# Kernel optimization log

Measured on AMD Instinct MI355X. Metric: run time of the kernel, lower is better.

The kernel has to match this reference:

```python
import jax, jax.numpy as jnp
import numpy as np

B = 128          # number of graphs
N = 512          # nodes per graph
D = 128          # input_dim == hid_dim
H = 128          # hid_dim
L = 2            # num GIN layers
E_PG = 8192      # edges per graph (avg degree 16)
OUT = 10
BN_EPS = 1e-5
RATIO = 0.5


def setup_inputs() -> dict:
    key = jax.random.key(0)
    ks = jax.random.split(key, 32)
    NT = B * N
    # per-graph random edges, offset into the global node index space
    e = jax.random.randint(ks[0], (2, B, E_PG), 0, N)
    offs = (jnp.arange(B) * N)[None, :, None]
    edge_index = (e + offs).reshape(2, -1).astype(jnp.int64)
    batch = jnp.repeat(jnp.arange(B), N).astype(jnp.int64)
    x = jax.random.normal(ks[1], (NT, D), dtype=jnp.float32)
    sc = 0.05
    inp = {
        'x': x, 'edge_index': edge_index, 'batch': batch,
        'epss': jax.random.normal(ks[2], (L,), jnp.float32) * 0.1,
        'Ws1': jax.random.normal(ks[3], (L, D, 2 * H), jnp.float32) * sc,
        'bs1': jax.random.normal(ks[4], (L, 2 * H), jnp.float32) * sc,
        'g1s': jax.random.uniform(ks[5], (L, 2 * H), jnp.float32, 0.5, 1.5),
        'be1s': jax.random.normal(ks[6], (L, 2 * H), jnp.float32) * sc,
        'rm1s': jax.random.normal(ks[7], (L, 2 * H), jnp.float32) * 0.1,
        'rv1s': jax.random.uniform(ks[8], (L, 2 * H), jnp.float32, 0.5, 1.5),
        'Ws2': jax.random.normal(ks[9], (L, 2 * H, H), jnp.float32) * sc,
        'bs2': jax.random.normal(ks[10], (L, H), jnp.float32) * sc,
        'gbn': jax.random.uniform(ks[11], (L, H), jnp.float32, 0.5, 1.5),
        'bbn': jax.random.normal(ks[12], (L, H), jnp.float32) * sc,
        'rmbn': jax.random.normal(ks[13], (L, H), jnp.float32) * 0.1,
        'rvbn': jax.random.uniform(ks[14], (L, H), jnp.float32, 0.5, 1.5),
        'Wrel': jax.random.normal(ks[15], (H, 1), jnp.float32) * sc,
        'brel': jax.random.normal(ks[16], (1,), jnp.float32) * sc,
        'Wroot': jax.random.normal(ks[17], (H, 1), jnp.float32) * sc,
        'W_lin1': jax.random.normal(ks[18], (H, H), jnp.float32) * sc,
        'b_lin1': jax.random.normal(ks[19], (H,), jnp.float32) * sc,
        'g_h': jax.random.uniform(ks[20], (H,), jnp.float32, 0.5, 1.5),
        'be_h': jax.random.normal(ks[21], (H,), jnp.float32) * sc,
        'rm_h': jax.random.normal(ks[22], (H,), jnp.float32) * 0.1,
        'rv_h': jax.random.uniform(ks[23], (H,), jnp.float32, 0.5, 1.5),
        'W_lin2': jax.random.normal(ks[24], (H, OUT), jnp.float32) * sc,
        'b_lin2': jax.random.normal(ks[25], (OUT,), jnp.float32) * sc,
    }
    return inp


def _bn(h, g, b, rm, rv):
    # eval-mode BatchNorm1d
    return (h - rm) * jax.lax.rsqrt(rv + BN_EPS) * g + b


def _forward(x, edge_index, batch, epss, Ws1, bs1, g1s, be1s, rm1s, rv1s,
             Ws2, bs2, gbn, bbn, rmbn, rvbn, Wrel, brel, Wroot,
             W_lin1, b_lin1, g_h, be_h, rm_h, rv_h, W_lin2, b_lin2):
    NT = x.shape[0]
    src, dst = edge_index[0], edge_index[1]
    # ---- stacked GINConv + BN + ReLU (eval: dropout = identity) ----
    for l in range(L):
        agg = jax.ops.segment_sum(x[src], dst, num_segments=NT)   # scatter-add
        h = (1.0 + epss[l]) * x + agg
        h = h @ Ws1[l] + bs1[l]
        h = jax.nn.relu(_bn(h, g1s[l], be1s[l], rm1s[l], rv1s[l]))
        h = h @ Ws2[l] + bs2[l]
        x = jax.nn.relu(_bn(h, gbn[l], bbn[l], rmbn[l], rvbn[l]))
    # ---- SAGPooling: GraphConv score -> tanh -> per-graph top-k ----
    agg = jax.ops.segment_sum(x[src], dst, num_segments=NT)
    score = (agg @ Wrel + brel + x @ Wroot)[:, 0]                 # [NT]
    s = jnp.tanh(score)
    K = int(np.ceil(RATIO * N))
    vals, idx = jax.lax.top_k(s.reshape(B, N), K)                 # [B,K]
    perm = (idx + (jnp.arange(B) * N)[:, None]).reshape(-1)       # global node ids
    x_pool = x[perm] * vals.reshape(-1)[:, None]                  # [B*K, H]
    batch_pool = batch[perm]
    # ---- global add pool ----
    embedding = jax.ops.segment_sum(x_pool, batch_pool, num_segments=B)  # [B,H]
    # ---- head (B > 1 branch) ----
    h = _bn(embedding @ W_lin1 + b_lin1, g_h, be_h, rm_h, rv_h)
    h = jax.nn.relu(h)
    logits = h @ W_lin2 + b_lin2
    return embedding, logits


def reference(x, edge_index, batch, epss, Ws1, bs1, g1s, be1s, rm1s, rv1s,
              Ws2, bs2, gbn, bbn, rmbn, rvbn, Wrel, brel, Wroot,
              W_lin1, b_lin1, g_h, be_h, rm_h, rv_h, W_lin2, b_lin2):
    return _forward(x, edge_index, batch, epss, Ws1, bs1, g1s, be1s, rm1s,
                    rv1s, Ws2, bs2, gbn, bbn, rmbn, rvbn, Wrel, brel, Wroot,
                    W_lin1, b_lin1, g_h, be_h, rm_h, rv_h, W_lin2, b_lin2)
```

## Files before the change

kernel.cpp:

```cpp
#include <hip/hip_runtime.h>
#include <hip/hip_bf16.h>
#include <stdint.h>
#include <math.h>

#define NT_ 65536
#define BGRAPH 128
#define NNODE 512
#define DIM 128
#define HID 128
#define H2 256
#define EDGES 1048576
#define EPG 8192
#define KSEL 256
#define OUTC 10

typedef float v2f __attribute__((ext_vector_type(2)));

__global__ __launch_bounds__(512) void k_csr(const int* __restrict__ src, const int* __restrict__ dst,
                                             int* __restrict__ row_start, int* __restrict__ csr2) {
    __shared__ int hist[512];
    __shared__ int scan_s[512];
    __shared__ int cur[512];
    __shared__ int eids[EPG];
    const int g = blockIdx.x;
    const int t = threadIdx.x;
    const int base = g * EPG;
    const int nb = g * NNODE;
    hist[t] = 0;
    __syncthreads();
    #pragma unroll
    for (int j = t; j < EPG; j += 512) {
        int d = dst[base + j] - nb;
        atomicAdd(&hist[d], 1);
    }
    __syncthreads();
    int v = hist[t];
    scan_s[t] = v;
    __syncthreads();
    for (int off = 1; off < 512; off <<= 1) {
        int u = (t >= off) ? scan_s[t - off] : 0;
        __syncthreads();
        scan_s[t] += u;
        __syncthreads();
    }
    int excl = scan_s[t] - v;
    row_start[nb + t] = base + excl;
    cur[t] = excl;
    if (g == BGRAPH - 1 && t == 511) row_start[NT_] = EDGES;
    __syncthreads();
    #pragma unroll
    for (int j = t; j < EPG; j += 512) {
        int d = dst[base + j] - nb;
        int pos = atomicAdd(&cur[d], 1);
        eids[pos] = (d << 16) | j;
    }
    __syncthreads();
    #pragma unroll
    for (int p = t; p < EPG; p += 512) {
        int packed = eids[p];
        int j = packed & 0xFFFF;
        int d = packed >> 16;
        int beg = scan_s[d] - hist[d];
        int end = scan_s[d];
        int rank = 0;
        for (int q = beg; q < end; ++q) rank += (int)((eids[q] & 0xFFFF) < j);
        csr2[base + beg + rank] = src[base + j];
    }
}

__global__ __launch_bounds__(256) void k_aggcomb(const float* __restrict__ X,
        const int* __restrict__ row_start, const int* __restrict__ csr_src,
        const float* __restrict__ epss, int l, float* __restrict__ XIN) {
    int bid = blockIdx.x;
    int wg = (bid & 7) * 1024 + (bid >> 3);
    int wave = threadIdx.x >> 6;
    int lane = threadIdx.x & 63;
    int half = lane >> 5;
    int l32 = lane & 31;
    int n = wg * 8 + wave * 2 + half;
    int beg = row_start[n], end = row_start[n + 1];
    const size_t co = (size_t)(l32 * 4);
    const float ep = __fadd_rn(1.0f, epss[l]);
    float a0 = 0.f, a1 = 0.f, a2 = 0.f, a3 = 0.f;
    int p = beg;
    for (; p + 8 <= end; p += 8) {
        int n0 = csr_src[p+0], n1 = csr_src[p+1], n2 = csr_src[p+2], n3 = csr_src[p+3];
        int n4 = csr_src[p+4], n5 = csr_src[p+5], n6 = csr_src[p+6], n7 = csr_src[p+7];
        float4 v0 = *(const float4*)(X + (size_t)n0 * DIM + co);
        float4 v1 = *(const float4*)(X + (size_t)n1 * DIM + co);
        float4 v2 = *(const float4*)(X + (size_t)n2 * DIM + co);
        float4 v3 = *(const float4*)(X + (size_t)n3 * DIM + co);
        float4 v4 = *(const float4*)(X + (size_t)n4 * DIM + co);
        float4 v5 = *(const float4*)(X + (size_t)n5 * DIM + co);
        float4 v6 = *(const float4*)(X + (size_t)n6 * DIM + co);
        float4 v7 = *(const float4*)(X + (size_t)n7 * DIM + co);
        a0 = __fadd_rn(a0, v0.x); a1 = __fadd_rn(a1, v0.y); a2 = __fadd_rn(a2, v0.z); a3 = __fadd_rn(a3, v0.w);
        a0 = __fadd_rn(a0, v1.x); a1 = __fadd_rn(a1, v1.y); a2 = __fadd_rn(a2, v1.z); a3 = __fadd_rn(a3, v1.w);
        a0 = __fadd_rn(a0, v2.x); a1 = __fadd_rn(a1, v2.y); a2 = __fadd_rn(a2, v2.z); a3 = __fadd_rn(a3, v2.w);
        a0 = __fadd_rn(a0, v3.x); a1 = __fadd_rn(a1, v3.y); a2 = __fadd_rn(a2, v3.z); a3 = __fadd_rn(a3, v3.w);
        a0 = __fadd_rn(a0, v4.x); a1 = __fadd_rn(a1, v4.y); a2 = __fadd_rn(a2, v4.z); a3 = __fadd_rn(a3, v4.w);
        a0 = __fadd_rn(a0, v5.x); a1 = __fadd_rn(a1, v5.y); a2 = __fadd_rn(a2, v5.z); a3 = __fadd_rn(a3, v5.w);
        a0 = __fadd_rn(a0, v6.x); a1 = __fadd_rn(a1, v6.y); a2 = __fadd_rn(a2, v6.z); a3 = __fadd_rn(a3, v6.w);
        a0 = __fadd_rn(a0, v7.x); a1 = __fadd_rn(a1, v7.y); a2 = __fadd_rn(a2, v7.z); a3 = __fadd_rn(a3, v7.w);
    }
    for (; p < end; ++p) {
        int nbr = csr_src[p];
        float4 v = *(const float4*)(X + (size_t)nbr * DIM + co);
        a0 = __fadd_rn(a0, v.x); a1 = __fadd_rn(a1, v.y); a2 = __fadd_rn(a2, v.z); a3 = __fadd_rn(a3, v.w);
    }
    float4 xv = *(const float4*)(X + (size_t)n * DIM + co);
    float4 o;
    o.x = __fadd_rn(__fmul_rn(ep, xv.x), a0);
    o.y = __fadd_rn(__fmul_rn(ep, xv.y), a1);
    o.z = __fadd_rn(__fmul_rn(ep, xv.z), a2);
    o.w = __fadd_rn(__fmul_rn(ep, xv.w), a3);
    *(float4*)(XIN + (size_t)n * DIM + co) = o;
}

__global__ __launch_bounds__(256) void k_gemm1(const float* __restrict__ XIN,
        const float* __restrict__ Ws1, const float* __restrict__ bs1,
        const float* __restrict__ g1s, const float* __restrict__ be1s, const float* __restrict__ rm1s,
        const float* __restrict__ rv1s, int l, float* __restrict__ H1out) {
    __shared__ float As[2][16][132];
    __shared__ float Bs[2][16][132];
    const float* W1  = Ws1 + (size_t)l * DIM * H2;
    const float* b1  = bs1 + l * H2;
    const float* g1  = g1s + l * H2;
    const float* be1 = be1s + l * H2;
    const float* rm1 = rm1s + l * H2;
    const float* rv1 = rv1s + l * H2;
    int bid = blockIdx.x;
    int wg = (bid & 7) * 128 + (bid >> 3);
    const int mbase = (wg >> 1) * 128;
    const int nbase = (wg & 1) * 128;
    const int tid = threadIdx.x;
    const int srow = tid >> 1;
    const int sk   = (tid & 1) * 8;
    const int bk   = tid >> 4;
    const int bc   = (tid & 15) * 4;
    const int ty = tid >> 4;
    const int tx = tid & 15;
    v2f acc[8][4] = {};
    const float* xr = XIN + (size_t)(mbase + srow) * DIM + sk;
    float4 px0, px1, pw0, pw1;
    px0 = *(const float4*)(xr);     px1 = *(const float4*)(xr + 4);
    {
        const float* wrow = W1 + (size_t)bk * H2 + nbase;
        pw0 = *(const float4*)(wrow + bc); pw1 = *(const float4*)(wrow + bc + 64);
    }
    As[0][sk + 0][srow] = px0.x;
    As[0][sk + 1][srow] = px0.y;
    As[0][sk + 2][srow] = px0.z;
    As[0][sk + 3][srow] = px0.w;
    As[0][sk + 4][srow] = px1.x;
    As[0][sk + 5][srow] = px1.y;
    As[0][sk + 6][srow] = px1.z;
    As[0][sk + 7][srow] = px1.w;
    *(float4*)&Bs[0][bk][bc]      = pw0;
    *(float4*)&Bs[0][bk][bc + 64] = pw1;
    __syncthreads();
    int cur = 0;
    for (int kt = 0; kt < DIM; kt += 16) {
        const int nxt = kt + 16;
        if (nxt < DIM) {
            px0 = *(const float4*)(xr + nxt);     px1 = *(const float4*)(xr + nxt + 4);
            const float* wrow = W1 + (size_t)(nxt + bk) * H2 + nbase;
            pw0 = *(const float4*)(wrow + bc); pw1 = *(const float4*)(wrow + bc + 64);
        }
        #pragma unroll
        for (int kk = 0; kk < 16; ++kk) {
            const float4 aA = *(const float4*)&As[cur][kk][ty * 8];
            const float4 aB = *(const float4*)&As[cur][kk][ty * 8 + 4];
            const float4 b0 = *(const float4*)&Bs[cur][kk][tx * 4];
            const float4 b1v = *(const float4*)&Bs[cur][kk][tx * 4 + 64];
            v2f b00; b00[0] = b0.x;  b00[1] = b0.y;
            v2f b01; b01[0] = b0.z;  b01[1] = b0.w;
            v2f b10; b10[0] = b1v.x; b10[1] = b1v.y;
            v2f b11; b11[0] = b1v.z; b11[1] = b1v.w;
            const float arr[8] = {aA.x, aA.y, aA.z, aA.w, aB.x, aB.y, aB.z, aB.w};
            #pragma unroll
            for (int i = 0; i < 8; ++i) {
                v2f ai; ai[0] = arr[i]; ai[1] = arr[i];
                acc[i][0] = __builtin_elementwise_fma(ai, b00, acc[i][0]);
                acc[i][1] = __builtin_elementwise_fma(ai, b01, acc[i][1]);
                acc[i][2] = __builtin_elementwise_fma(ai, b10, acc[i][2]);
                acc[i][3] = __builtin_elementwise_fma(ai, b11, acc[i][3]);
            }
        }
        if (nxt < DIM) {
            const int nb = cur ^ 1;
            As[nb][sk + 0][srow] = px0.x;
            As[nb][sk + 1][srow] = px0.y;
            As[nb][sk + 2][srow] = px0.z;
            As[nb][sk + 3][srow] = px0.w;
            As[nb][sk + 4][srow] = px1.x;
            As[nb][sk + 5][srow] = px1.y;
            As[nb][sk + 6][srow] = px1.z;
            As[nb][sk + 7][srow] = px1.w;
            *(float4*)&Bs[nb][bk][bc]      = pw0;
            *(float4*)&Bs[nb][bk][bc + 64] = pw1;
            __syncthreads();
        }
        cur ^= 1;
    }
    const int gc = nbase + tx * 4;
    float bb[8], iv[8], gg[8], rr[8], ee[8];
    #pragma unroll
    for (int j = 0; j < 8; ++j) {
        int c = (j < 4) ? (gc + j) : (gc + 60 + j);
        bb[j] = b1[c];
        iv[j] = __fdiv_rn(1.0f, __fsqrt_rn(__fadd_rn(rv1[c], 1e-5f)));
        gg[j] = g1[c];
        rr[j] = rm1[c];
        ee[j] = be1[c];
    }
    #pragma unroll
    for (int i = 0; i < 8; ++i) {
        const int gr = mbase + ty * 8 + i;
        float cv[8] = {acc[i][0][0], acc[i][0][1], acc[i][1][0], acc[i][1][1],
                       acc[i][2][0], acc[i][2][1], acc[i][3][0], acc[i][3][1]};
        float r[8];
        #pragma unroll
        for (int j = 0; j < 8; ++j) {
            float t = __fadd_rn(cv[j], bb[j]);
            t = __fsub_rn(t, rr[j]); t = __fmul_rn(t, iv[j]);
            t = __fmul_rn(t, gg[j]); t = __fadd_rn(t, ee[j]);
            r[j] = fmaxf(t, 0.f);
        }
        float4 o0; o0.x = r[0]; o0.y = r[1]; o0.z = r[2]; o0.w = r[3];
        float4 o1; o1.x = r[4]; o1.y = r[5]; o1.z = r[6]; o1.w = r[7];
        *(float4*)(H1out + (size_t)gr * H2 + gc)      = o0;
        *(float4*)(H1out + (size_t)gr * H2 + gc + 64) = o1;
    }
}

__global__ __launch_bounds__(256) void k_gemm2(const float* __restrict__ H1, const float* __restrict__ Ws2,
        const float* __restrict__ bs2, const float* __restrict__ gbn, const float* __restrict__ bbn,
        const float* __restrict__ rmbn, const float* __restrict__ rvbn, int l, float* __restrict__ Xout) {
    __shared__ float As[2][16][132];
    __shared__ float Bs[2][16][132];
    const float* W2 = Ws2 + (size_t)l * H2 * HID;
    const float* b2 = bs2 + l * HID;
    const float* g  = gbn + l * HID;
    const float* be = bbn + l * HID;
    const float* rm = rmbn + l * HID;
    const float* rv = rvbn + l * HID;
    int bid = blockIdx.x;
    int wg = (bid & 7) * 64 + (bid >> 3);
    const int mbase = wg * 128;
    const int tid = threadIdx.x;
    const int srow = tid >> 1;
    const int sk   = (tid & 1) * 8;
    const int bk   = tid >> 4;
    const int bc   = (tid & 15) * 4;
    const int ty = tid >> 4;
    const int tx = tid & 15;
    v2f acc[8][4] = {};
    const float* hr = H1 + (size_t)(mbase + srow) * H2 + sk;
    float4 ph0, ph1, pw0, pw1;
    ph0 = *(const float4*)(hr);     ph1 = *(const float4*)(hr + 4);
    {
        const float* wrow = W2 + (size_t)bk * HID;
        pw0 = *(const float4*)(wrow + bc); pw1 = *(const float4*)(wrow + bc + 64);
    }
    As[0][sk + 0][srow] = ph0.x;
    As[0][sk + 1][srow] = ph0.y;
    As[0][sk + 2][srow] = ph0.z;
    As[0][sk + 3][srow] = ph0.w;
    As[0][sk + 4][srow] = ph1.x;
    As[0][sk + 5][srow] = ph1.y;
    As[0][sk + 6][srow] = ph1.z;
    As[0][sk + 7][srow] = ph1.w;
    *(float4*)&Bs[0][bk][bc]      = pw0;
    *(float4*)&Bs[0][bk][bc + 64] = pw1;
    __syncthreads();
    int cur = 0;
    for (int kt = 0; kt < H2; kt += 16) {
        const int nxt = kt + 16;
        if (nxt < H2) {
            ph0 = *(const float4*)(hr + nxt);     ph1 = *(const float4*)(hr + nxt + 4);
            const float* wrow = W2 + (size_t)(nxt + bk) * HID;
            pw0 = *(const float4*)(wrow + bc); pw1 = *(const float4*)(wrow + bc + 64);
        }
        #pragma unroll
        for (int kk = 0; kk < 16; ++kk) {
            const float4 aA = *(const float4*)&As[cur][kk][ty * 8];
            const float4 aB = *(const float4*)&As[cur][kk][ty * 8 + 4];
            const float4 b0 = *(const float4*)&Bs[cur][kk][tx * 4];
            const float4 b1v = *(const float4*)&Bs[cur][kk][tx * 4 + 64];
            v2f b00; b00[0] = b0.x;  b00[1] = b0.y;
            v2f b01; b01[0] = b0.z;  b01[1] = b0.w;
            v2f b10; b10[0] = b1v.x; b10[1] = b1v.y;
            v2f b11; b11[0] = b1v.z; b11[1] = b1v.w;
            const float arr[8] = {aA.x, aA.y, aA.z, aA.w, aB.x, aB.y, aB.z, aB.w};
            #pragma unroll
            for (int i = 0; i < 8; ++i) {
                v2f ai; ai[0] = arr[i]; ai[1] = arr[i];
                acc[i][0] = __builtin_elementwise_fma(ai, b00, acc[i][0]);
                acc[i][1] = __builtin_elementwise_fma(ai, b01, acc[i][1]);
                acc[i][2] = __builtin_elementwise_fma(ai, b10, acc[i][2]);
                acc[i][3] = __builtin_elementwise_fma(ai, b11, acc[i][3]);
            }
        }
        if (nxt < H2) {
            const int nb = cur ^ 1;
            As[nb][sk + 0][srow] = ph0.x;
            As[nb][sk + 1][srow] = ph0.y;
            As[nb][sk + 2][srow] = ph0.z;
            As[nb][sk + 3][srow] = ph0.w;
            As[nb][sk + 4][srow] = ph1.x;
            As[nb][sk + 5][srow] = ph1.y;
            As[nb][sk + 6][srow] = ph1.z;
            As[nb][sk + 7][srow] = ph1.w;
            *(float4*)&Bs[nb][bk][bc]      = pw0;
            *(float4*)&Bs[nb][bk][bc + 64] = pw1;
            __syncthreads();
        }
        cur ^= 1;
    }
    const int gc = tx * 4;
    float bb[8], iv[8], gg[8], rr[8], ee[8];
    #pragma unroll
    for (int j = 0; j < 8; ++j) {
        int c = (j < 4) ? (gc + j) : (gc + 60 + j);
        bb[j] = b2[c];
        iv[j] = __fdiv_rn(1.0f, __fsqrt_rn(__fadd_rn(rv[c], 1e-5f)));
        gg[j] = g[c];
        rr[j] = rm[c];
        ee[j] = be[c];
    }
    #pragma unroll
    for (int i = 0; i < 8; ++i) {
        const int gr = mbase + ty * 8 + i;
        float cv[8] = {acc[i][0][0], acc[i][0][1], acc[i][1][0], acc[i][1][1],
                       acc[i][2][0], acc[i][2][1], acc[i][3][0], acc[i][3][1]};
        float r[8];
        #pragma unroll
        for (int j = 0; j < 8; ++j) {
            float t = __fadd_rn(cv[j], bb[j]);
            t = __fsub_rn(t, rr[j]); t = __fmul_rn(t, iv[j]);
            t = __fmul_rn(t, gg[j]); t = __fadd_rn(t, ee[j]);
            r[j] = fmaxf(t, 0.f);
        }
        float4 o0; o0.x = r[0]; o0.y = r[1]; o0.z = r[2]; o0.w = r[3];
        float4 o1; o1.x = r[4]; o1.y = r[5]; o1.z = r[6]; o1.w = r[7];
        *(float4*)(Xout + (size_t)gr * HID + gc)      = o0;
        *(float4*)(Xout + (size_t)gr * HID + gc + 64) = o1;
    }
}

__global__ __launch_bounds__(256) void k_aggscore(const float* __restrict__ X,
        const int* __restrict__ row_start, const int* __restrict__ csr_src,
        const float* __restrict__ Wrel, const float* __restrict__ brel,
        const float* __restrict__ Wroot, float* __restrict__ S) {
    int bid = blockIdx.x;
    int wg = (bid & 7) * 1024 + (bid >> 3);
    int wave = threadIdx.x >> 6;
    int lane = threadIdx.x & 63;
    int half = lane >> 5;
    int l32 = lane & 31;
    int n = wg * 8 + wave * 2 + half;
    int beg = row_start[n], end = row_start[n + 1];
    const size_t co = (size_t)(l32 * 4);
    float a0 = 0.f, a1 = 0.f, a2 = 0.f, a3 = 0.f;
    int p = beg;
    for (; p + 8 <= end; p += 8) {
        int n0 = csr_src[p+0], n1 = csr_src[p+1], n2 = csr_src[p+2], n3 = csr_src[p+3];
        int n4 = csr_src[p+4], n5 = csr_src[p+5], n6 = csr_src[p+6], n7 = csr_src[p+7];
        float4 v0 = *(const float4*)(X + (size_t)n0 * DIM + co);
        float4 v1 = *(const float4*)(X + (size_t)n1 * DIM + co);
        float4 v2 = *(const float4*)(X + (size_t)n2 * DIM + co);
        float4 v3 = *(const float4*)(X + (size_t)n3 * DIM + co);
        float4 v4 = *(const float4*)(X + (size_t)n4 * DIM + co);
        float4 v5 = *(const float4*)(X + (size_t)n5 * DIM + co);
        float4 v6 = *(const float4*)(X + (size_t)n6 * DIM + co);
        float4 v7 = *(const float4*)(X + (size_t)n7 * DIM + co);
        a0 = __fadd_rn(a0, v0.x); a1 = __fadd_rn(a1, v0.y); a2 = __fadd_rn(a2, v0.z); a3 = __fadd_rn(a3, v0.w);
        a0 = __fadd_rn(a0, v1.x); a1 = __fadd_rn(a1, v1.y); a2 = __fadd_rn(a2, v1.z); a3 = __fadd_rn(a3, v1.w);
        a0 = __fadd_rn(a0, v2.x); a1 = __fadd_rn(a1, v2.y); a2 = __fadd_rn(a2, v2.z); a3 = __fadd_rn(a3, v2.w);
        a0 = __fadd_rn(a0, v3.x); a1 = __fadd_rn(a1, v3.y); a2 = __fadd_rn(a2, v3.z); a3 = __fadd_rn(a3, v3.w);
        a0 = __fadd_rn(a0, v4.x); a1 = __fadd_rn(a1, v4.y); a2 = __fadd_rn(a2, v4.z); a3 = __fadd_rn(a3, v4.w);
        a0 = __fadd_rn(a0, v5.x); a1 = __fadd_rn(a1, v5.y); a2 = __fadd_rn(a2, v5.z); a3 = __fadd_rn(a3, v5.w);
        a0 = __fadd_rn(a0, v6.x); a1 = __fadd_rn(a1, v6.y); a2 = __fadd_rn(a2, v6.z); a3 = __fadd_rn(a3, v6.w);
        a0 = __fadd_rn(a0, v7.x); a1 = __fadd_rn(a1, v7.y); a2 = __fadd_rn(a2, v7.z); a3 = __fadd_rn(a3, v7.w);
    }
    for (; p < end; ++p) {
        int nbr = csr_src[p];
        float4 v = *(const float4*)(X + (size_t)nbr * DIM + co);
        a0 = __fadd_rn(a0, v.x); a1 = __fadd_rn(a1, v.y); a2 = __fadd_rn(a2, v.z); a3 = __fadd_rn(a3, v.w);
    }
    float4 xv  = *(const float4*)(X + (size_t)n * DIM + co);
    float4 wrv = *(const float4*)(Wrel + co);
    float4 wov = *(const float4*)(Wroot + co);
    float p1 = __fmul_rn(a0, wrv.x);
    p1 = __fmaf_rn(a1, wrv.y, p1);
    p1 = __fmaf_rn(a2, wrv.z, p1);
    p1 = __fmaf_rn(a3, wrv.w, p1);
    float p2 = __fmul_rn(xv.x, wov.x);
    p2 = __fmaf_rn(xv.y, wov.y, p2);
    p2 = __fmaf_rn(xv.z, wov.z, p2);
    p2 = __fmaf_rn(xv.w, wov.w, p2);
    #pragma unroll
    for (int off = 1; off <= 16; off <<= 1) {
        p1 += __shfl_xor(p1, off);
        p2 += __shfl_xor(p2, off);
    }
    if (l32 == 0) {
        float pp = __fadd_rn(__fadd_rn(p1, brel[0]), p2);
        const float PC = 7.90531110763549805f;
        float s;
        if (pp >= PC)       s = 1.0f;
        else if (pp <= -PC) s = -1.0f;
        else                s = (float)tanh((double)pp);
        S[n] = s;
    }
}

__global__ __launch_bounds__(512) void k_pool(const float* __restrict__ X, const float* __restrict__ S,
                                              float* __restrict__ EMB, double* __restrict__ EMB64) {
    __shared__ unsigned key[512];
    __shared__ double w[512];
    __shared__ double red[4][128];
    const int b = blockIdx.x, tid = threadIdx.x;
    float v = S[b * NNODE + tid];
    unsigned u = __float_as_uint(v);
    unsigned o = (u & 0x80000000u) ? ~u : (u | 0x80000000u);
    key[tid] = o;
    __syncthreads();
    int rank = 0;
    for (int j = 0; j < NNODE; ++j) {
        unsigned kj = key[j];
        rank += (int)((kj > o) || (kj == o && j < tid));
    }
    w[tid] = (rank < KSEL) ? (double)v : 0.0;
    __syncthreads();
    const int jgrp = tid >> 7;
    const int col = tid & 127;
    double acc = 0.0;
    for (int i = jgrp; i < NNODE; i += 4) {
        acc += (double)X[((size_t)b * NNODE + i) * HID + col] * w[i];
    }
    red[jgrp][col] = acc;
    __syncthreads();
    if (jgrp == 0) {
        double e = red[0][col] + red[1][col] + red[2][col] + red[3][col];
        EMB[b * HID + col] = (float)e;
        EMB64[b * HID + col] = e;
    }
}

__global__ __launch_bounds__(128) void k_head(const double* __restrict__ EMB64,
        const float* __restrict__ W1, const float* __restrict__ b1,
        const float* __restrict__ g, const float* __restrict__ be,
        const float* __restrict__ rm, const float* __restrict__ rv,
        const float* __restrict__ W2, const float* __restrict__ b2,
        float* __restrict__ LOGITS) {
    __shared__ double e[128];
    __shared__ double h[128];
    const int b = blockIdx.x, t = threadIdx.x;
    e[t] = EMB64[b * HID + t];
    __syncthreads();
    double acc = 0.0;
    for (int k = 0; k < HID; ++k) acc += e[k] * (double)W1[k * HID + t];
    acc += (double)b1[t];
    double inv = 1.0 / sqrt((double)rv[t] + 1e-5);
    acc = (acc - (double)rm[t]) * inv * (double)g[t] + (double)be[t];
    h[t] = fmax(acc, 0.0);
    __syncthreads();
    if (t < OUTC) {
        double a2 = (double)b2[t];
        for (int k = 0; k < HID; ++k) a2 += h[k] * (double)W2[k * OUTC + t];
        LOGITS[b * OUTC + t] = (float)a2;
    }
}

extern "C" void kernel_launch(void* const* d_in, const int* in_sizes, int n_in,
                              void* d_out, int out_size, void* d_ws, size_t ws_size,
                              hipStream_t stream) {
    const float* x     = (const float*)d_in[0];
    const int*   edge  = (const int*)d_in[1];
    const int*   src   = edge;
    const int*   dst   = edge + EDGES;
    const float* epss  = (const float*)d_in[3];
    const float* Ws1   = (const float*)d_in[4];
    const float* bs1   = (const float*)d_in[5];
    const float* g1s   = (const float*)d_in[6];
    const float* be1s  = (const float*)d_in[7];
    const float* rm1s  = (const float*)d_in[8];
    const float* rv1s  = (const float*)d_in[9];
    const float* Ws2   = (const float*)d_in[10];
    const float* bs2   = (const float*)d_in[11];
    const float* gbn   = (const float*)d_in[12];
    const float* bbn   = (const float*)d_in[13];
    const float* rmbn  = (const float*)d_in[14];
    const float* rvbn  = (const float*)d_in[15];
    const float* Wrel  = (const float*)d_in[16];
    const float* brel  = (const float*)d_in[17];
    const float* Wroot = (const float*)d_in[18];
    const float* W_lin1= (const float*)d_in[19];
    const float* b_lin1= (const float*)d_in[20];
    const float* g_h   = (const float*)d_in[21];
    const float* be_h  = (const float*)d_in[22];
    const float* rm_h  = (const float*)d_in[23];
    const float* rv_h  = (const float*)d_in[24];
    const float* W_lin2= (const float*)d_in[25];
    const float* b_lin2= (const float*)d_in[26];

    char* ws = (char*)d_ws;
    float*  x_cur    = (float*) (ws);
    float*  xin      = (float*) (ws + 33554432);
    float*  h1       = (float*) (ws + 67108864);
    float*  s32      = (float*) (ws + 134217728);
    double* emb64    = (double*)(ws + 134479872);
    int*    row_start= (int*)   (ws + 134610944);
    int*    csr2     = (int*)   (ws + 134897664);

    float* emb    = (float*)d_out;
    float* logits = (float*)d_out + BGRAPH * HID;

    k_csr<<<BGRAPH, 512, 0, stream>>>(src, dst, row_start, csr2);

    k_aggcomb<<<NT_ / 8, 256, 0, stream>>>(x, row_start, csr2, epss, 0, xin);
    k_gemm1<<<1024, 256, 0, stream>>>(xin, Ws1, bs1, g1s, be1s, rm1s, rv1s, 0, h1);
    k_gemm2<<<512, 256, 0, stream>>>(h1, Ws2, bs2, gbn, bbn, rmbn, rvbn, 0, x_cur);
    k_aggcomb<<<NT_ / 8, 256, 0, stream>>>(x_cur, row_start, csr2, epss, 1, xin);
    k_gemm1<<<1024, 256, 0, stream>>>(xin, Ws1, bs1, g1s, be1s, rm1s, rv1s, 1, h1);
    k_gemm2<<<512, 256, 0, stream>>>(h1, Ws2, bs2, gbn, bbn, rmbn, rvbn, 1, x_cur);
    k_aggscore<<<NT_ / 8, 256, 0, stream>>>(x_cur, row_start, csr2, Wrel, brel, Wroot, s32);
    k_pool<<<BGRAPH, 512, 0, stream>>>(x_cur, s32, emb, emb64);
    k_head<<<BGRAPH, 128, 0, stream>>>(emb64, W_lin1, b_lin1, g_h, be_h, rm_h, rv_h, W_lin2, b_lin2, logits);
}
```

Before: 408.0 us.

## Project node features onto Wrel before aggregation in the score stage

The pooling score agg@Wrel is linear, so the change computes each node's dot products with Wrel and Wroot first and then aggregates the per-node scalar over neighbours. This replaces a gather of full 128-wide feature rows per edge with a gather of one float per edge. It adds a second small kernel launch. It also changes the floating-point summation order relative to the reference, which could perturb scores near top-k ties.

After: 393.6 us. -3.5%, faster.

```diff
diff --git a/kernel.cpp b/kernel.cpp
--- a/kernel.cpp
+++ b/kernel.cpp
@@ -349,71 +349,39 @@
     }
 }
 
-__global__ __launch_bounds__(256) void k_aggscore(const float* __restrict__ X,
-        const int* __restrict__ row_start, const int* __restrict__ csr_src,
-        const float* __restrict__ Wrel, const float* __restrict__ brel,
-        const float* __restrict__ Wroot, float* __restrict__ S) {
-    int bid = blockIdx.x;
-    int wg = (bid & 7) * 1024 + (bid >> 3);
+__global__ __launch_bounds__(256) void k_ydot(const float* __restrict__ X,
+        const float* __restrict__ Wrel, const float* __restrict__ Wroot,
+        float* __restrict__ Y, float* __restrict__ Z) {
     int wave = threadIdx.x >> 6;
     int lane = threadIdx.x & 63;
-    int half = lane >> 5;
-    int l32 = lane & 31;
-    int n = wg * 8 + wave * 2 + half;
-    int beg = row_start[n], end = row_start[n + 1];
-    const size_t co = (size_t)(l32 * 4);
-    float a0 = 0.f, a1 = 0.f, a2 = 0.f, a3 = 0.f;
-    int p = beg;
-    for (; p + 8 <= end; p += 8) {
-        int n0 = csr_src[p+0], n1 = csr_src[p+1], n2 = csr_src[p+2], n3 = csr_src[p+3];
-        int n4 = csr_src[p+4], n5 = csr_src[p+5], n6 = csr_src[p+6], n7 = csr_src[p+7];
-        float4 v0 = *(const float4*)(X + (size_t)n0 * DIM + co);
-        float4 v1 = *(const float4*)(X + (size_t)n1 * DIM + co);
-        float4 v2 = *(const float4*)(X + (size_t)n2 * DIM + co);
-        float4 v3 = *(const float4*)(X + (size_t)n3 * DIM + co);
-        float4 v4 = *(const float4*)(X + (size_t)n4 * DIM + co);
-        float4 v5 = *(const float4*)(X + (size_t)n5 * DIM + co);
-        float4 v6 = *(const float4*)(X + (size_t)n6 * DIM + co);
-        float4 v7 = *(const float4*)(X + (size_t)n7 * DIM + co);
-        a0 = __fadd_rn(a0, v0.x); a1 = __fadd_rn(a1, v0.y); a2 = __fadd_rn(a2, v0.z); a3 = __fadd_rn(a3, v0.w);
-        a0 = __fadd_rn(a0, v1.x); a1 = __fadd_rn(a1, v1.y); a2 = __fadd_rn(a2, v1.z); a3 = __fadd_rn(a3, v1.w);
-        a0 = __fadd_rn(a0, v2.x); a1 = __fadd_rn(a1, v2.y); a2 = __fadd_rn(a2, v2.z); a3 = __fadd_rn(a3, v2.w);
-        a0 = __fadd_rn(a0, v3.x); a1 = __fadd_rn(a1, v3.y); a2 = __fadd_rn(a2, v3.z); a3 = __fadd_rn(a3, v3.w);
-        a0 = __fadd_rn(a0, v4.x); a1 = __fadd_rn(a1, v4.y); a2 = __fadd_rn(a2, v4.z); a3 = __fadd_rn(a3, v4.w);
-        a0 = __fadd_rn(a0, v5.x); a1 = __fadd_rn(a1, v5.y); a2 = __fadd_rn(a2, v5.z); a3 = __fadd_rn(a3, v5.w);
-        a0 = __fadd_rn(a0, v6.x); a1 = __fadd_rn(a1, v6.y); a2 = __fadd_rn(a2, v6.z); a3 = __fadd_rn(a3, v6.w);
-        a0 = __fadd_rn(a0, v7.x); a1 = __fadd_rn(a1, v7.y); a2 = __fadd_rn(a2, v7.z); a3 = __fadd_rn(a3, v7.w);
-    }
-    for (; p < end; ++p) {
-        int nbr = csr_src[p];
-        float4 v = *(const float4*)(X + (size_t)nbr * DIM + co);
-        a0 = __fadd_rn(a0, v.x); a1 = __fadd_rn(a1, v.y); a2 = __fadd_rn(a2, v.z); a3 = __fadd_rn(a3, v.w);
-    }
-    float4 xv  = *(const float4*)(X + (size_t)n * DIM + co);
-    float4 wrv = *(const float4*)(Wrel + co);
-    float4 wov = *(const float4*)(Wroot + co);
-    float p1 = __fmul_rn(a0, wrv.x);
-    p1 = __fmaf_rn(a1, wrv.y, p1);
-    p1 = __fmaf_rn(a2, wrv.z, p1);
-    p1 = __fmaf_rn(a3, wrv.w, p1);
-    float p2 = __fmul_rn(xv.x, wov.x);
-    p2 = __fmaf_rn(xv.y, wov.y, p2);
-    p2 = __fmaf_rn(xv.z, wov.z, p2);
-    p2 = __fmaf_rn(xv.w, wov.w, p2);
-    #pragma unroll
-    for (int off = 1; off <= 16; off <<= 1) {
+    int n = blockIdx.x * 4 + wave;
+    const float2 xv = *(const float2*)(X + (size_t)n * HID + lane * 2);
+    const float2 wr = *(const float2*)(Wrel + lane * 2);
+    const float2 wo = *(const float2*)(Wroot + lane * 2);
+    float p1 = __fmaf_rn(xv.y, wr.y, __fmul_rn(xv.x, wr.x));
+    float p2 = __fmaf_rn(xv.y, wo.y, __fmul_rn(xv.x, wo.x));
+    #pragma unroll
+    for (int off = 1; off <= 32; off <<= 1) {
         p1 += __shfl_xor(p1, off);
         p2 += __shfl_xor(p2, off);
     }
-    if (l32 == 0) {
-        float pp = __fadd_rn(__fadd_rn(p1, brel[0]), p2);
-        const float PC = 7.90531110763549805f;
-        float s;
-        if (pp >= PC)       s = 1.0f;
-        else if (pp <= -PC) s = -1.0f;
-        else                s = (float)tanh((double)pp);
-        S[n] = s;
-    }
+    if (lane == 0) { Y[n] = p1; Z[n] = p2; }
+}
+
+__global__ __launch_bounds__(256) void k_scorelite(const float* __restrict__ Y, const float* __restrict__ Z,
+        const int* __restrict__ row_start, const int* __restrict__ csr_src,
+        const float* __restrict__ brel, float* __restrict__ S) {
+    int n = blockIdx.x * 256 + threadIdx.x;
+    int beg = row_start[n], end = row_start[n + 1];
+    float p1 = 0.f;
+    for (int p = beg; p < end; ++p) p1 = __fadd_rn(p1, Y[csr_src[p]]);
+    float pp = __fadd_rn(__fadd_rn(p1, brel[0]), Z[n]);
+    const float PC = 7.90531110763549805f;
+    float s;
+    if (pp >= PC)       s = 1.0f;
+    else if (pp <= -PC) s = -1.0f;
+    else                s = (float)tanh((double)pp);
+    S[n] = s;
 }
 
 __global__ __launch_bounds__(512) void k_pool(const float* __restrict__ X, const float* __restrict__ S,
@@ -511,9 +479,11 @@
     float*  xin      = (float*) (ws + 33554432);
     float*  h1       = (float*) (ws + 67108864);
     float*  s32      = (float*) (ws + 134217728);
-    double* emb64    = (double*)(ws + 134479872);
-    int*    row_start= (int*)   (ws + 134610944);
-    int*    csr2     = (int*)   (ws + 134897664);
+    float*  ybuf     = (float*) (ws + 134479872);
+    float*  zbuf     = (float*) (ws + 134742016);
+    double* emb64    = (double*)(ws + 135004160);
+    int*    row_start= (int*)   (ws + 135135232);
+    int*    csr2     = (int*)   (ws + 135421952);
 
     float* emb    = (float*)d_out;
     float* logits = (float*)d_out + BGRAPH * HID;
@@ -526,7 +496,8 @@
     k_aggcomb<<<NT_ / 8, 256, 0, stream>>>(x_cur, row_start, csr2, epss, 1, xin);
     k_gemm1<<<1024, 256, 0, stream>>>(xin, Ws1, bs1, g1s, be1s, rm1s, rv1s, 1, h1);
     k_gemm2<<<512, 256, 0, stream>>>(h1, Ws2, bs2, gbn, bbn, rmbn, rvbn, 1, x_cur);
-    k_aggscore<<<NT_ / 8, 256, 0, stream>>>(x_cur, row_start, csr2, Wrel, brel, Wroot, s32);
+    k_ydot<<<NT_ / 4, 256, 0, stream>>>(x_cur, Wrel, Wroot, ybuf, zbuf);
+    k_scorelite<<<NT_ / 256, 256, 0, stream>>>(ybuf, zbuf, row_start, csr2, brel, s32);
     k_pool<<<BGRAPH, 512, 0, stream>>>(x_cur, s32, emb, emb64);
     k_head<<<BGRAPH, 128, 0, stream>>>(emb64, W_lin1, b_lin1, g_h, be_h, rm_h, rv_h, W_lin2, b_lin2, logits);
 }
```
